# Performance work log

Hardware: AMD Instinct MI355X
Metric: run time of the kernel (lower is better)

Reference implementation:

```python
import jax, jax.numpy as jnp
import numpy as np

O, I = 4096, 4096          # out_features, in_features
N = 8192                   # tokens (batch*seq)
ROW_BS, COL_BS = 1, 4      # block sparsity granularity
ZP_OUT = 0                 # output zero point (int)
QMIN, QMAX = -128.0, 127.0 # qint8 range


def setup_inputs() -> dict:
    key = jax.random.key(0)
    k1, k2, k3, k4 = jax.random.split(key, 4)
    # dequantized fp32 activations
    x = jax.random.normal(k1, (N, I), dtype=jnp.float32)
    # int8 weight values (zero point 0), stored as float32 integers in [-127,127]
    w_q = jnp.round(jnp.clip(jax.random.normal(k2, (O, I), dtype=jnp.float32) * 40.0, QMIN + 1, QMAX))
    bias = jax.random.normal(k3, (O,), dtype=jnp.float32) * 0.1
    block_mask = jax.random.randint(k4, (O // ROW_BS, I // COL_BS), 0, 2, dtype=jnp.int32)
    w_scale = jnp.float32(0.01)   # per-tensor weight scale, weight zp == 0
    out_scale = jnp.float32(0.05) # activation (output) quant scale
    return {"x": x, "w_q": w_q, "bias": bias, "w_scale": w_scale,
            "out_scale": out_scale, "block_mask": block_mask}


def reference(x, w_q, bias, w_scale, out_scale, block_mask):
    # expand block mask to element mask [O, I]
    m = jnp.repeat(jnp.repeat(block_mask, ROW_BS, axis=0), COL_BS, axis=1).astype(w_q.dtype)
    w_eff = w_q * m                                  # masked int8 weight values
    # dequantized GEMM: (x @ W^T) * w_scale + bias
    y = jnp.einsum('ni,oi->no', x, w_eff) * w_scale + bias  # [N, O]
    # quantize output to qint8 (scale=out_scale, zp=ZP_OUT), return dequantized repr
    q = jnp.clip(jnp.round(y / out_scale) + ZP_OUT, QMIN, QMAX)
    return (q - ZP_OUT) * out_scale
```

## Files before the change

### kernel.cpp

```cpp
#include <hip/hip_runtime.h>


#define M_TOK 8192
#define O_FEAT 4096
#define K_FEAT 4096

#define BM 256
#define BN 256
#define BK 64
#define NT (K_FEAT / BK)

using f16x8 = __attribute__((ext_vector_type(8))) _Float16;
using f32x4 = __attribute__((ext_vector_type(4))) float;

#define BAR()    asm volatile("s_barrier" ::: "memory")
#define VMCNT(n) asm volatile("s_waitcnt vmcnt(" #n ")" ::: "memory")
#define MFMA16(a, b, c) __builtin_amdgcn_mfma_f32_16x16x32_f16((a), (b), (c), 0, 0, 0)

__global__ __launch_bounds__(256) void cvt_x_kernel(const float* __restrict__ x,
                                                    _Float16* __restrict__ xf) {
    size_t i = ((size_t)blockIdx.x * 256 + threadIdx.x) * 8;
    float4 v0 = *reinterpret_cast<const float4*>(x + i);
    float4 v1 = *reinterpret_cast<const float4*>(x + i + 4);
    f16x8 h;
    h[0] = (_Float16)v0.x; h[1] = (_Float16)v0.y;
    h[2] = (_Float16)v0.z; h[3] = (_Float16)v0.w;
    h[4] = (_Float16)v1.x; h[5] = (_Float16)v1.y;
    h[6] = (_Float16)v1.z; h[7] = (_Float16)v1.w;
    *reinterpret_cast<f16x8*>(xf + i) = h;
}

__global__ __launch_bounds__(256) void cvt_w_kernel(const float* __restrict__ wq,
                                                    const int* __restrict__ mask,
                                                    _Float16* __restrict__ wf) {
    size_t i = ((size_t)blockIdx.x * 256 + threadIdx.x) * 8;
    float4 v0 = *reinterpret_cast<const float4*>(wq + i);
    float4 v1 = *reinterpret_cast<const float4*>(wq + i + 4);
    int2 mv = *reinterpret_cast<const int2*>(mask + i / 4);
    float m0 = mv.x ? 1.0f : 0.0f;
    float m1 = mv.y ? 1.0f : 0.0f;
    f16x8 h;
    h[0] = (_Float16)(v0.x * m0); h[1] = (_Float16)(v0.y * m0);
    h[2] = (_Float16)(v0.z * m0); h[3] = (_Float16)(v0.w * m0);
    h[4] = (_Float16)(v1.x * m1); h[5] = (_Float16)(v1.y * m1);
    h[6] = (_Float16)(v1.z * m1); h[7] = (_Float16)(v1.w * m1);
    *reinterpret_cast<f16x8*>(wf + i) = h;
}

__global__ __launch_bounds__(512, 2) void gemm_kernel(const _Float16* __restrict__ A,
                                                      const _Float16* __restrict__ B,
                                                      const float* __restrict__ bias,
                                                      const float* __restrict__ wsp,
                                                      const float* __restrict__ osp,
                                                      float* __restrict__ C) {
    __shared__ __align__(16) _Float16 smem[2][2][2][BM * 32];

    const int tid  = threadIdx.x;
    const int lane = tid & 63;
    const int w    = tid >> 6;
    const int wm   = w >> 2;
    const int wn   = w & 3;
    const int lr   = lane & 15;
    const int kq   = lane >> 4;

    const int bm = blockIdx.x >> 4;
    const int bn = blockIdx.x & 15;

    const _Float16* Abase = A + (size_t)(bm * BM) * K_FEAT;
    const _Float16* Bbase = B + (size_t)(bn * BN) * K_FEAT;

    const int sr0  = w * 32 + (lane >> 2);
    const int csrc = (((lane & 3) ^ ((lane >> 3) & 3))) * 8;

    auto stage = [&](int buf, int mat, int kh, const _Float16* gbase, int t) {
#pragma unroll
        for (int j = 0; j < 2; ++j) {
            const int r = sr0 + j * 16;
            const _Float16* src = gbase + (size_t)r * K_FEAT + t * BK + kh * 32 + csrc;
            _Float16* dst = &smem[buf][mat][kh][(w * 128 + j * 64 + lane) * 8];
            __builtin_amdgcn_global_load_lds(
                (const __attribute__((address_space(1))) void*)(const void*)src,
                (__attribute__((address_space(3))) void*)(void*)dst, 16, 0, 0);
        }
    };
    auto lda = [&](int buf, int kh, int m) -> f16x8 {
        const int r = wm * 128 + m * 16 + lr;
        return *reinterpret_cast<const f16x8*>(
            &smem[buf][0][kh][r * 32 + ((kq ^ ((r >> 1) & 3)) << 3)]);
    };
    auto ldb = [&](int buf, int kh, int n) -> f16x8 {
        const int r = wn * 64 + n * 16 + lr;
        return *reinterpret_cast<const f16x8*>(
            &smem[buf][1][kh][r * 32 + ((kq ^ ((r >> 1) & 3)) << 3)]);
    };

    f32x4 acc[8][4] = {};
    f16x8 a0[4], a1[4], b0[4], b1[4];

    stage(0, 0, 0, Abase, 0);
    stage(0, 1, 0, Bbase, 0);
    VMCNT(0);
    BAR();
#pragma unroll
    for (int m = 0; m < 4; ++m) a0[m] = lda(0, 0, m);
#pragma unroll
    for (int n = 0; n < 4; ++n) b0[n] = ldb(0, 0, n);
    stage(0, 0, 1, Abase, 0);
    stage(0, 1, 1, Bbase, 0);

    for (int s = 0; s < NT; ++s) {
        const int b  = s & 1;
        const int nb = b ^ 1;

#pragma unroll
        for (int m = 0; m < 4; ++m) a1[m] = lda(b, 0, 4 + m);
        if (s + 1 < NT) stage(nb, 0, 0, Abase, s + 1);
        BAR();
        __builtin_amdgcn_s_setprio(1);
#pragma unroll
        for (int m = 0; m < 4; ++m)
#pragma unroll
            for (int n = 0; n < 4; ++n)
                acc[m][n] = MFMA16(a0[m], b0[n], acc[m][n]);
        __builtin_amdgcn_s_setprio(0);
        if (s == NT - 1) { VMCNT(0); } else { VMCNT(2); }
        BAR();

#pragma unroll
        for (int m = 0; m < 4; ++m) a0[m] = lda(b, 1, m);
#pragma unroll
        for (int n = 0; n < 4; ++n) b1[n] = ldb(b, 1, n);
        if (s + 1 < NT) stage(nb, 1, 0, Bbase, s + 1);
        BAR();
        __builtin_amdgcn_s_setprio(1);
#pragma unroll
        for (int m = 0; m < 4; ++m)
#pragma unroll
            for (int n = 0; n < 4; ++n)
                acc[4 + m][n] = MFMA16(a1[m], b0[n], acc[4 + m][n]);
        __builtin_amdgcn_s_setprio(0);

#pragma unroll
        for (int m = 0; m < 4; ++m) a1[m] = lda(b, 1, 4 + m);
        if (s + 1 < NT) stage(nb, 0, 1, Abase, s + 1);
        BAR();
        __builtin_amdgcn_s_setprio(1);
#pragma unroll
        for (int m = 0; m < 4; ++m)
#pragma unroll
            for (int n = 0; n < 4; ++n)
                acc[m][n] = MFMA16(a0[m], b1[n], acc[m][n]);
        __builtin_amdgcn_s_setprio(0);
        if (s + 1 < NT) { VMCNT(2); BAR(); }

        if (s + 1 < NT) {
#pragma unroll
            for (int m = 0; m < 4; ++m) a0[m] = lda(nb, 0, m);
#pragma unroll
            for (int n = 0; n < 4; ++n) b0[n] = ldb(nb, 0, n);
            stage(nb, 1, 1, Bbase, s + 1);
        }
        BAR();
        __builtin_amdgcn_s_setprio(1);
#pragma unroll
        for (int m = 0; m < 4; ++m)
#pragma unroll
            for (int n = 0; n < 4; ++n)
                acc[4 + m][n] = MFMA16(a1[m], b1[n], acc[4 + m][n]);
        __builtin_amdgcn_s_setprio(0);
    }

    const float wscale = wsp[0];
    const float oscale = osp[0];
    const int row0 = bm * BM + wm * 128;
    const int col0 = bn * BN + wn * 64;
#pragma unroll
    for (int n = 0; n < 4; ++n) {
        const int col = col0 + n * 16 + lr;
        const float bc = bias[col];
#pragma unroll
        for (int m = 0; m < 8; ++m) {
#pragma unroll
            for (int j = 0; j < 4; ++j) {
                const int row = row0 + m * 16 + kq * 4 + j;
                float y = acc[m][n][j] * wscale + bc;
                float q = rintf(y / oscale);
                q = fminf(fmaxf(q, -128.0f), 127.0f);
                C[(size_t)row * O_FEAT + col] = q * oscale;
            }
        }
    }
}

extern "C" void kernel_launch(void* const* d_in, const int* in_sizes, int n_in,
                              void* d_out, int out_size, void* d_ws, size_t ws_size,
                              hipStream_t stream) {
    const float* x        = (const float*)d_in[0];
    const float* wq       = (const float*)d_in[1];
    const float* bias     = (const float*)d_in[2];
    const float* w_scale  = (const float*)d_in[3];
    const float* out_scale= (const float*)d_in[4];
    const int*   mask     = (const int*)d_in[5];
    float* out = (float*)d_out;

    _Float16* xf = (_Float16*)d_ws;
    _Float16* wf = (_Float16*)((char*)d_ws + (size_t)M_TOK * K_FEAT * 2);

    cvt_x_kernel<<<(M_TOK * (size_t)K_FEAT) / 8 / 256, 256, 0, stream>>>(x, xf);
    cvt_w_kernel<<<(O_FEAT * (size_t)K_FEAT) / 8 / 256, 256, 0, stream>>>(wq, mask, wf);

    gemm_kernel<<<dim3((M_TOK / BM) * (O_FEAT / BN)), 512, 0, stream>>>(
        xf, wf, bias, w_scale, out_scale, out);
}
```

Baseline: 300.2 us.

## Restructure GEMM staging into paired half-tile loads with precomputed LDS offsets and block swizzle

The GEMM main loop now issues global-to-LDS loads in two batches of A+B per k-half instead of four separate stages. LDS read offsets are precomputed and pointer increments replace per-iteration address math. Block indices are also swizzled so neighbouring workgroups are spread over different output tiles, aiming at better L2 reuse. The vmcnt waits are adjusted to match the new load grouping, which changes how much load latency overlaps with MFMA work.

```diff
diff --git a/kernel.cpp b/kernel.cpp
--- a/kernel.cpp
+++ b/kernel.cpp
@@ -9,6 +9,10 @@
 #define BN 256
 #define BK 64
 #define NT (K_FEAT / BK)
+
+#define S_BUF 32768
+#define S_MAT 16384
+#define S_KH  8192
 
 using f16x8 = __attribute__((ext_vector_type(8))) _Float16;
 using f32x4 = __attribute__((ext_vector_type(4))) float;
@@ -54,6 +58,7 @@
                                                       const float* __restrict__ osp,
                                                       float* __restrict__ C) {
     __shared__ __align__(16) _Float16 smem[2][2][2][BM * 32];
+    _Float16* sm = &smem[0][0][0][0];
 
     const int tid  = threadIdx.x;
     const int lane = tid & 63;
@@ -63,110 +68,123 @@
     const int lr   = lane & 15;
     const int kq   = lane >> 4;
 
-    const int bm = blockIdx.x >> 4;
-    const int bn = blockIdx.x & 15;
-
-    const _Float16* Abase = A + (size_t)(bm * BM) * K_FEAT;
-    const _Float16* Bbase = B + (size_t)(bn * BN) * K_FEAT;
+    const int swz = ((blockIdx.x & 7) << 6) | (blockIdx.x >> 3);
+    const int bm = swz >> 4;
+    const int bn = swz & 15;
 
     const int sr0  = w * 32 + (lane >> 2);
-    const int csrc = (((lane & 3) ^ ((lane >> 3) & 3))) * 8;
-
-    auto stage = [&](int buf, int mat, int kh, const _Float16* gbase, int t) {
-#pragma unroll
-        for (int j = 0; j < 2; ++j) {
-            const int r = sr0 + j * 16;
-            const _Float16* src = gbase + (size_t)r * K_FEAT + t * BK + kh * 32 + csrc;
-            _Float16* dst = &smem[buf][mat][kh][(w * 128 + j * 64 + lane) * 8];
-            __builtin_amdgcn_global_load_lds(
-                (const __attribute__((address_space(1))) void*)(const void*)src,
-                (__attribute__((address_space(3))) void*)(void*)dst, 16, 0, 0);
-        }
+    const int csrc = ((lane & 3) ^ ((lane >> 3) & 3)) * 8;
+    const size_t J1 = (size_t)16 * K_FEAT;
+
+    const _Float16* pA0 = A + (size_t)(bm * BM + sr0) * K_FEAT + csrc;
+    const _Float16* pA1 = pA0 + 32;
+    const _Float16* pB0 = B + (size_t)(bn * BN + sr0) * K_FEAT + csrc;
+    const _Float16* pB1 = pB0 + 32;
+
+    const int dst0 = (w * 128 + lane) * 8;
+    const int dst1 = dst0 + 64 * 8;
+
+    auto stg = [&](const _Float16* src, _Float16* dstp) {
+        __builtin_amdgcn_global_load_lds(
+            (const __attribute__((address_space(1))) void*)(const void*)src,
+            (__attribute__((address_space(3))) void*)(void*)dstp, 16, 0, 0);
     };
-    auto lda = [&](int buf, int kh, int m) -> f16x8 {
+
+    int offA[4], offB[4];
+#pragma unroll
+    for (int m = 0; m < 4; ++m) {
         const int r = wm * 128 + m * 16 + lr;
-        return *reinterpret_cast<const f16x8*>(
-            &smem[buf][0][kh][r * 32 + ((kq ^ ((r >> 1) & 3)) << 3)]);
+        offA[m] = r * 32 + ((kq ^ ((r >> 1) & 3)) << 3);
+    }
+#pragma unroll
+    for (int n = 0; n < 4; ++n) {
+        const int r = wn * 64 + n * 16 + lr;
+        offB[n] = r * 32 + ((kq ^ ((r >> 1) & 3)) << 3);
+    }
+    auto rd = [&](const _Float16* sbuf, int off, int immE) -> f16x8 {
+        return *reinterpret_cast<const f16x8*>(sbuf + off + immE);
     };
-    auto ldb = [&](int buf, int kh, int n) -> f16x8 {
-        const int r = wn * 64 + n * 16 + lr;
-        return *reinterpret_cast<const f16x8*>(
-            &smem[buf][1][kh][r * 32 + ((kq ^ ((r >> 1) & 3)) << 3)]);
-    };
 
     f32x4 acc[8][4] = {};
-    f16x8 a0[4], a1[4], b0[4], b1[4];
-
-    stage(0, 0, 0, Abase, 0);
-    stage(0, 1, 0, Bbase, 0);
-    VMCNT(0);
+    f16x8 a0[4], a1[4], b0v[4], b1v[4];
+
+    stg(pA0, sm + dst0);                    stg(pA0 + J1, sm + dst1);
+    stg(pB0, sm + S_MAT + dst0);            stg(pB0 + J1, sm + S_MAT + dst1);
+    stg(pA1, sm + S_KH + dst0);             stg(pA1 + J1, sm + S_KH + dst1);
+    stg(pB1, sm + S_MAT + S_KH + dst0);     stg(pB1 + J1, sm + S_MAT + S_KH + dst1);
+    VMCNT(4);
     BAR();
 #pragma unroll
-    for (int m = 0; m < 4; ++m) a0[m] = lda(0, 0, m);
-#pragma unroll
-    for (int n = 0; n < 4; ++n) b0[n] = ldb(0, 0, n);
-    stage(0, 0, 1, Abase, 0);
-    stage(0, 1, 1, Bbase, 0);
+    for (int m = 0; m < 4; ++m) a0[m] = rd(sm, offA[m], 0);
+#pragma unroll
+    for (int n = 0; n < 4; ++n) b0v[n] = rd(sm, offB[n], S_MAT);
+    pA0 += BK; pA1 += BK; pB0 += BK; pB1 += BK;
 
     for (int s = 0; s < NT; ++s) {
-        const int b  = s & 1;
-        const int nb = b ^ 1;
-
-#pragma unroll
-        for (int m = 0; m < 4; ++m) a1[m] = lda(b, 0, 4 + m);
-        if (s + 1 < NT) stage(nb, 0, 0, Abase, s + 1);
-        BAR();
-        __builtin_amdgcn_s_setprio(1);
-#pragma unroll
-        for (int m = 0; m < 4; ++m)
-#pragma unroll
-            for (int n = 0; n < 4; ++n)
-                acc[m][n] = MFMA16(a0[m], b0[n], acc[m][n]);
-        __builtin_amdgcn_s_setprio(0);
-        if (s == NT - 1) { VMCNT(0); } else { VMCNT(2); }
-        BAR();
-
-#pragma unroll
-        for (int m = 0; m < 4; ++m) a0[m] = lda(b, 1, m);
-#pragma unroll
-        for (int n = 0; n < 4; ++n) b1[n] = ldb(b, 1, n);
-        if (s + 1 < NT) stage(nb, 1, 0, Bbase, s + 1);
-        BAR();
-        __builtin_amdgcn_s_setprio(1);
-#pragma unroll
-        for (int m = 0; m < 4; ++m)
-#pragma unroll
-            for (int n = 0; n < 4; ++n)
-                acc[4 + m][n] = MFMA16(a1[m], b0[n], acc[4 + m][n]);
-        __builtin_amdgcn_s_setprio(0);
-
-#pragma unroll
-        for (int m = 0; m < 4; ++m) a1[m] = lda(b, 1, 4 + m);
-        if (s + 1 < NT) stage(nb, 0, 1, Abase, s + 1);
-        BAR();
-        __builtin_amdgcn_s_setprio(1);
-#pragma unroll
-        for (int m = 0; m < 4; ++m)
-#pragma unroll
-            for (int n = 0; n < 4; ++n)
-                acc[m][n] = MFMA16(a0[m], b1[n], acc[m][n]);
-        __builtin_amdgcn_s_setprio(0);
-        if (s + 1 < NT) { VMCNT(2); BAR(); }
-
-        if (s + 1 < NT) {
-#pragma unroll
-            for (int m = 0; m < 4; ++m) a0[m] = lda(nb, 0, m);
-#pragma unroll
-            for (int n = 0; n < 4; ++n) b0[n] = ldb(nb, 0, n);
-            stage(nb, 1, 1, Bbase, s + 1);
-        }
-        BAR();
-        __builtin_amdgcn_s_setprio(1);
-#pragma unroll
-        for (int m = 0; m < 4; ++m)
-#pragma unroll
-            for (int n = 0; n < 4; ++n)
-                acc[4 + m][n] = MFMA16(a1[m], b1[n], acc[4 + m][n]);
+        const _Float16* sb = sm + ((s & 1) ? S_BUF : 0);
+        _Float16*       sn = sm + ((s & 1) ? 0 : S_BUF);
+        const bool more = (s + 1 < NT);
+
+#pragma unroll
+        for (int m = 0; m < 4; ++m) a1[m] = rd(sb, offA[m], 2048);
+        if (more) {
+            stg(pA0, sn + dst0);            stg(pA0 + J1, sn + dst1);
+            stg(pB0, sn + S_MAT + dst0);    stg(pB0 + J1, sn + S_MAT + dst1);
+        }
+        BAR();
+        __builtin_amdgcn_s_setprio(1);
+#pragma unroll
+        for (int m = 0; m < 4; ++m)
+#pragma unroll
+            for (int n = 0; n < 4; ++n)
+                acc[m][n] = MFMA16(a0[m], b0v[n], acc[m][n]);
+        __builtin_amdgcn_s_setprio(0);
+        if (s == NT - 1) { VMCNT(0); } else { VMCNT(4); }
+        BAR();
+
+#pragma unroll
+        for (int m = 0; m < 4; ++m) a0[m] = rd(sb, offA[m], S_KH);
+#pragma unroll
+        for (int n = 0; n < 4; ++n) b1v[n] = rd(sb, offB[n], S_MAT + S_KH);
+        BAR();
+        __builtin_amdgcn_s_setprio(1);
+#pragma unroll
+        for (int m = 0; m < 4; ++m)
+#pragma unroll
+            for (int n = 0; n < 4; ++n)
+                acc[4 + m][n] = MFMA16(a1[m], b0v[n], acc[4 + m][n]);
+        __builtin_amdgcn_s_setprio(0);
+
+#pragma unroll
+        for (int m = 0; m < 4; ++m) a1[m] = rd(sb, offA[m], S_KH + 2048);
+        if (more) {
+            stg(pA1, sn + S_KH + dst0);          stg(pA1 + J1, sn + S_KH + dst1);
+            stg(pB1, sn + S_MAT + S_KH + dst0);  stg(pB1 + J1, sn + S_MAT + S_KH + dst1);
+        }
+        BAR();
+        __builtin_amdgcn_s_setprio(1);
+#pragma unroll
+        for (int m = 0; m < 4; ++m)
+#pragma unroll
+            for (int n = 0; n < 4; ++n)
+                acc[m][n] = MFMA16(a0[m], b1v[n], acc[m][n]);
+        __builtin_amdgcn_s_setprio(0);
+        if (more) { VMCNT(4); BAR(); }
+
+        if (more) {
+#pragma unroll
+            for (int m = 0; m < 4; ++m) a0[m] = rd(sn, offA[m], 0);
+#pragma unroll
+            for (int n = 0; n < 4; ++n) b0v[n] = rd(sn, offB[n], S_MAT);
+            pA0 += BK; pA1 += BK; pB0 += BK; pB1 += BK;
+        }
+        BAR();
+        __builtin_amdgcn_s_setprio(1);
+#pragma unroll
+        for (int m = 0; m < 4; ++m)
+#pragma unroll
+            for (int n = 0; n < 4; ++n)
+                acc[4 + m][n] = MFMA16(a1[m], b1v[n], acc[4 + m][n]);
         __builtin_amdgcn_s_setprio(0);
     }
 
```

After: 342.2 us. 14.0% more time.
